# Optimization experiments

Hardware: AMD Instinct MI355X
Metric: run time of the kernel (lower is better)

## Reference

```python
import jax, jax.numpy as jnp
import numpy as np

NEG_SLOPE = 0.2
EPS = 1e-16


def gat_conv(x, edge_index, W, att_src, att_dst, bias, heads, out_ch, concat):
    """PyG GATConv (eval mode, add_self_loops=True).
    x: [N, F_in], edge_index: [2, E] with row0=src(j), row1=dst(i).
    W: [F_in, heads*out_ch], att_src/att_dst: [heads, out_ch], bias: [heads*out_ch] or [out_ch].
    """
    N = x.shape[0]
    loop = jnp.arange(N, dtype=edge_index.dtype)
    src = jnp.concatenate([edge_index[0], loop])
    dst = jnp.concatenate([edge_index[1], loop])

    h = (x @ W).reshape(N, heads, out_ch)                 # [N, H, C]
    a_src = jnp.sum(h * att_src[None], axis=-1)           # [N, H]
    a_dst = jnp.sum(h * att_dst[None], axis=-1)           # [N, H]

    alpha = jax.nn.leaky_relu(a_src[src] + a_dst[dst], NEG_SLOPE)  # [E, H]
    # segment softmax over incoming edges of each destination node
    m = jax.ops.segment_max(alpha, dst, num_segments=N)   # [N, H]
    e = jnp.exp(alpha - m[dst])                           # [E, H]
    s = jax.ops.segment_sum(e, dst, num_segments=N)       # [N, H]
    alpha = e / (s[dst] + EPS)                            # [E, H]

    out = jax.ops.segment_sum(h[src] * alpha[:, :, None], dst, num_segments=N)  # [N, H, C]
    if concat:
        out = out.reshape(N, heads * out_ch)
    else:
        out = out.mean(axis=1)
    return out + bias


def setup_inputs() -> dict:
    key = jax.random.key(0)
    ks = jax.random.split(key, 12)
    N, E, F_in, C = 100000, 1600000, 512, 16
    H1, O1 = 8, 8
    hid = H1 * O1  # 64
    sc1 = 1.0 / np.sqrt(F_in)
    sc2 = 1.0 / np.sqrt(hid)
    return {
        "x": jax.random.normal(ks[0], (N, F_in), jnp.float32),
        "edge_index": jax.random.randint(ks[1], (2, E), 0, N, jnp.int64),
        "W1": jax.random.normal(ks[2], (F_in, hid), jnp.float32) * sc1,
        "att_src1": jax.random.normal(ks[3], (H1, O1), jnp.float32) * sc2,
        "att_dst1": jax.random.normal(ks[4], (H1, O1), jnp.float32) * sc2,
        "bias1": jnp.zeros((hid,), jnp.float32),
        "W2": jax.random.normal(ks[5], (hid, C), jnp.float32) * sc2,
        "att_src2": jax.random.normal(ks[6], (1, C), jnp.float32) * 0.25,
        "att_dst2": jax.random.normal(ks[7], (1, C), jnp.float32) * 0.25,
        "bias2": jnp.zeros((C,), jnp.float32),
    }


def reference(x, edge_index, W1, att_src1, att_dst1, bias1, W2, att_src2, att_dst2, bias2):
    h = gat_conv(x, edge_index, W1, att_src1, att_dst1, bias1, heads=8, out_ch=8, concat=True)
    h = jax.nn.elu(h)
    C = W2.shape[1]
    node_embeddings = gat_conv(h, edge_index, W2, att_src2, att_dst2, bias2, heads=1, out_ch=C, concat=True)
    out = jax.nn.softmax(node_embeddings, axis=-1)
    return (out, node_embeddings)
```

## Files before the change

kernel.cpp:

```cpp
#include <hip/hip_runtime.h>
#include <hip/hip_bf16.h>

#define NEG_SLOPE 0.2f
#define EPSF 1e-16f

typedef __attribute__((ext_vector_type(8))) short bf16x8;
typedef __attribute__((ext_vector_type(4))) float f32x4;

__device__ inline unsigned short f2bf(float x) {
  unsigned int u = __float_as_uint(x);
  return (unsigned short)((u + 0x7fffu + ((u >> 16) & 1u)) >> 16);
}
__device__ inline float bf2f(unsigned short h) {
  return __uint_as_float(((unsigned int)h) << 16);
}

__device__ __forceinline__ void gload16(const void* src, void* dst) {
  __builtin_amdgcn_global_load_lds(
      (const __attribute__((address_space(1))) unsigned int*)src,
      (__attribute__((address_space(3))) unsigned int*)dst, 16, 0, 0);
}

__global__ __launch_bounds__(256) void prep_w_kernel(const float* __restrict__ W,
                                                     unsigned short* __restrict__ wb) {
  int idx = blockIdx.x * 256 + threadIdx.x;
  if (idx >= 512 * 64) return;
  int k = idx >> 6, c = idx & 63;
  float w = W[idx];
  unsigned short h = f2bf(w);
  unsigned short l = f2bf(w - bf2f(h));
  int ch = k >> 5, kin = k & 31;
  int Ap = ((c << 6) + (kin << 1)) ^ ((c & 7) << 4);
  wb[ch * 4096 + (Ap >> 1)] = h;
  wb[ch * 4096 + 2048 + (Ap >> 1)] = l;
}

__global__ __launch_bounds__(256) void gemm1_kernel(const float* __restrict__ x,
                                                    const unsigned short* __restrict__ wb,
                                                    const float* __restrict__ atts,
                                                    const float* __restrict__ attd,
                                                    unsigned short* __restrict__ h1b,
                                                    float* __restrict__ a1s,
                                                    float* __restrict__ a1d, int N) {
  __shared__ __align__(16) float As[3][4096];
  __shared__ __align__(16) unsigned short Bs[3][4096];
  const int tid = threadIdx.x, wv = tid >> 6, lane = tid & 63;
  const int row0 = blockIdx.x * 128;

  const float* asrc[4];
  int aldo[4];
#pragma unroll
  for (int i = 0; i < 4; ++i) {
    int u = i * 256 + wv * 64 + lane;
    int row = u >> 3, w = u & 7;
    int rg = row0 + row;
    if (rg >= N) rg = N - 1;
    asrc[i] = x + (size_t)rg * 512 + ((w ^ (row & 7)) << 2);
    aldo[i] = (i * 256 + wv * 64) * 4;
  }
  const unsigned short* bsrc[2];
  int bldo[2];
#pragma unroll
  for (int i = 0; i < 2; ++i) {
    int u = i * 256 + wv * 64 + lane;
    bsrc[i] = wb + (size_t)u * 8;
    bldo[i] = (i * 256 + wv * 64) * 8;
  }

  const int kofs = (lane >> 4) * 8;
  const int cbase = lane & 15;
  int ardo[2][2];
#pragma unroll
  for (int rt = 0; rt < 2; ++rt) {
    int r = wv * 32 + rt * 16 + cbase;
#pragma unroll
    for (int h = 0; h < 2; ++h)
      ardo[rt][h] = r * 32 + ((((kofs >> 2) + h) ^ (r & 7)) << 2);
  }
  int brdo[4];
#pragma unroll
  for (int ct = 0; ct < 4; ++ct) {
    int c = ct * 16 + cbase;
    brdo[ct] = (((c << 6) + (kofs << 1)) ^ ((c & 7) << 4)) >> 1;
  }

  f32x4 acc[2][4] = {};

  auto stage = [&](int b, int ch) {
#pragma unroll
    for (int i = 0; i < 4; ++i) gload16(asrc[i] + ch * 32, &As[b][aldo[i]]);
#pragma unroll
    for (int i = 0; i < 2; ++i) gload16(bsrc[i] + ch * 4096, &Bs[b][bldo[i]]);
  };

  stage(0, 0);
  stage(1, 1);
  for (int i = 0; i < 16; ++i) {
    const int b = i % 3;
    if (i < 14) {
      stage((i + 2) % 3, i + 2);
      asm volatile("s_waitcnt vmcnt(12)" ::: "memory");
    } else if (i == 14) {
      asm volatile("s_waitcnt vmcnt(6)" ::: "memory");
    } else {
      asm volatile("s_waitcnt vmcnt(0)" ::: "memory");
    }
    __builtin_amdgcn_s_barrier();
    __builtin_amdgcn_sched_barrier(0);

#pragma unroll
    for (int rt = 0; rt < 2; ++rt) {
      float4 a0 = *(const float4*)(&As[b][ardo[rt][0]]);
      float4 a1 = *(const float4*)(&As[b][ardo[rt][1]]);
      float av[8] = {a0.x, a0.y, a0.z, a0.w, a1.x, a1.y, a1.z, a1.w};
      bf16x8 ah, al;
#pragma unroll
      for (int j = 0; j < 8; ++j) {
        unsigned int u = __float_as_uint(av[j]);
        ah[j] = (short)(unsigned short)(u >> 16);
        float lo = av[j] - __uint_as_float(u & 0xffff0000u);
        al[j] = (short)(unsigned short)(__float_as_uint(lo) >> 16);
      }
#pragma unroll
      for (int ct = 0; ct < 4; ++ct) {
        bf16x8 bh = *(const bf16x8*)(&Bs[b][brdo[ct]]);
        bf16x8 bl = *(const bf16x8*)(&Bs[b][brdo[ct] + 2048]);
        acc[rt][ct] = __builtin_amdgcn_mfma_f32_16x16x32_bf16(ah, bh, acc[rt][ct], 0, 0, 0);
        acc[rt][ct] = __builtin_amdgcn_mfma_f32_16x16x32_bf16(al, bh, acc[rt][ct], 0, 0, 0);
        acc[rt][ct] = __builtin_amdgcn_mfma_f32_16x16x32_bf16(ah, bl, acc[rt][ct], 0, 0, 0);
      }
    }
    asm volatile("s_waitcnt lgkmcnt(0)" ::: "memory");
    __builtin_amdgcn_s_barrier();
  }

  float wS[4], wD[4];
#pragma unroll
  for (int ct = 0; ct < 4; ++ct) {
    wS[ct] = atts[ct * 16 + cbase];
    wD[ct] = attd[ct * 16 + cbase];
  }
#pragma unroll
  for (int rt = 0; rt < 2; ++rt) {
#pragma unroll
    for (int ct = 0; ct < 4; ++ct) {
#pragma unroll
      for (int j = 0; j < 4; ++j) {
        int r = row0 + wv * 32 + rt * 16 + (lane >> 4) * 4 + j;
        float a = acc[rt][ct][j];
        if (r < N) h1b[(size_t)r * 64 + ct * 16 + cbase] = f2bf(a);
        float ps = a * wS[ct], pd = a * wD[ct];
        ps += __shfl_xor(ps, 1); pd += __shfl_xor(pd, 1);
        ps += __shfl_xor(ps, 2); pd += __shfl_xor(pd, 2);
        ps += __shfl_xor(ps, 4); pd += __shfl_xor(pd, 4);
        if ((lane & 7) == 0 && r < N) {
          int h = ct * 2 + ((lane >> 3) & 1);
          a1s[r * 8 + h] = ps;
          a1d[r * 8 + h] = pd;
        }
      }
    }
  }
}

__global__ __launch_bounds__(256) void init_deg_kernel(int* __restrict__ deg, int N) {
  int i = blockIdx.x * 256 + threadIdx.x;
  if (i < N) deg[i] = 1;
}

__global__ __launch_bounds__(256) void count_kernel(const int* __restrict__ ei, int E, int* __restrict__ deg) {
  int e = blockIdx.x * 256 + threadIdx.x;
  if (e < E) atomicAdd(&deg[ei[E + e]], 1);
}

__global__ __launch_bounds__(256) void scan1_kernel(int* __restrict__ data, int* __restrict__ blocksum, int N) {
  __shared__ int wave_tot[4];
  int t = threadIdx.x;
  int base = blockIdx.x * 1024;
  int v[4];
  int sum = 0;
#pragma unroll
  for (int i = 0; i < 4; ++i) {
    int idx = base + t * 4 + i;
    v[i] = sum;
    int d = (idx < N) ? data[idx] : 0;
    sum += d;
  }
  int lane = t & 63, wv = t >> 6;
  int x = sum;
#pragma unroll
  for (int ofs = 1; ofs < 64; ofs <<= 1) {
    int y = __shfl_up(x, ofs);
    if (lane >= ofs) x += y;
  }
  if (lane == 63) wave_tot[wv] = x;
  __syncthreads();
  int wofs = 0;
  for (int w = 0; w < wv; ++w) wofs += wave_tot[w];
  int excl_thread = wofs + x - sum;
#pragma unroll
  for (int i = 0; i < 4; ++i) {
    int idx = base + t * 4 + i;
    if (idx < N) data[idx] = excl_thread + v[i];
  }
  if (t == 255) blocksum[blockIdx.x] = wofs + x;
}

__global__ __launch_bounds__(256) void scan2_kernel(int* __restrict__ blocksum, int nb) {
  __shared__ int sm[256];
  int t = threadIdx.x;
  int x = (t < nb) ? blocksum[t] : 0;
  sm[t] = x;
  __syncthreads();
  for (int ofs = 1; ofs < 256; ofs <<= 1) {
    int y = (t >= ofs) ? sm[t - ofs] : 0;
    __syncthreads();
    sm[t] += y;
    __syncthreads();
  }
  if (t < nb) blocksum[t] = sm[t] - x;
}

__global__ __launch_bounds__(256) void scan3_kernel(const int* __restrict__ excl, const int* __restrict__ blocksum,
                                                    int* __restrict__ rowptr, int* __restrict__ cursor,
                                                    int N, int ET) {
  int idx = blockIdx.x * 256 + threadIdx.x;
  if (idx < N) {
    int r = excl[idx] + blocksum[idx >> 10];
    rowptr[idx] = r;
    cursor[idx] = r;
  }
  if (idx == N) rowptr[N] = ET;
}

__global__ __launch_bounds__(256) void scatter_kernel(const int* __restrict__ ei, int E, int ET,
                                                      int* __restrict__ cursor, int* __restrict__ esrc, int N) {
  const int cls = blockIdx.x & 7;
  const int nlo = (int)(((long long)N * cls) >> 3);
  const int nhi = (int)(((long long)N * (cls + 1)) >> 3);
  const int chunk = blockIdx.x >> 3;
  const int nchunks = gridDim.x >> 3;
  const long long stride = (long long)nchunks * 256;
  for (long long e = (long long)chunk * 256 + threadIdx.x; e < ET; e += stride) {
    int s, d;
    if (e < E) { d = ei[E + e]; s = ei[e]; }
    else       { d = (int)(e - E); s = d; }
    if (d >= nlo && d < nhi) {
      int pos = atomicAdd(&cursor[d], 1);
      esrc[pos] = s;
    }
  }
}

__global__ __launch_bounds__(256) void agg1_kernel(const int* __restrict__ rowptr, const int* __restrict__ esrc,
                                                   const float* __restrict__ a1s, const float* __restrict__ a1d,
                                                   const unsigned short* __restrict__ h1b,
                                                   const float* __restrict__ bias1,
                                                   unsigned short* __restrict__ h2b, int N) {
  const int wid = (blockIdx.x * 256 + threadIdx.x) >> 6;
  const int lane = threadIdx.x & 63;
  const int half = lane >> 5, l = lane & 31;
  const int nA = wid * 2;
  if (nA >= N) return;
  const int n = nA + half;
  const bool nvalid = n < N;
  const int nc = nvalid ? n : nA;
  const int h = l >> 2;
  const int c2 = l * 2;

  const float ad = a1d[(unsigned)nc * 8 + h];
  const int beg = rowptr[nc];
  const int deg = nvalid ? (rowptr[nc + 1] - beg) : 0;
  const int degO = __shfl_xor(deg, 32);
  const int dmax = max(deg, degO);
  const int dcl = max(deg, 1) - 1;

  float acc0 = 0.f, acc1 = 0.f, wsum = 0.f;
  for (int it = 0; it < dmax; it += 2) {
    int k0 = beg + min(it, dcl);
    int k1 = beg + min(it + 1, dcl);
    float m0 = (it < deg) ? 1.f : 0.f;
    float m1 = (it + 1 < deg) ? 1.f : 0.f;
    int s0 = esrc[k0], s1 = esrc[k1];
    unsigned int g0 = *(const unsigned int*)(h1b + ((unsigned)s0 * 64 + c2));
    unsigned int g1 = *(const unsigned int*)(h1b + ((unsigned)s1 * 64 + c2));
    float al0 = a1s[(unsigned)s0 * 8 + h] + ad;
    float al1 = a1s[(unsigned)s1 * 8 + h] + ad;
    al0 = fmaxf(al0, NEG_SLOPE * al0);
    al1 = fmaxf(al1, NEG_SLOPE * al1);
    float w0 = __expf(al0) * m0;
    float w1 = __expf(al1) * m1;
    acc0 = fmaf(w0, bf2f((unsigned short)(g0 & 0xffff)), acc0);
    acc1 = fmaf(w0, bf2f((unsigned short)(g0 >> 16)), acc1);
    acc0 = fmaf(w1, bf2f((unsigned short)(g1 & 0xffff)), acc0);
    acc1 = fmaf(w1, bf2f((unsigned short)(g1 >> 16)), acc1);
    wsum += w0 + w1;
  }
  float inv = 1.f / (wsum + EPSF);
  float2 b2 = *(const float2*)(bias1 + c2);
  float v0 = acc0 * inv + b2.x;
  float v1 = acc1 * inv + b2.y;
  v0 = (v0 > 0.f) ? v0 : expm1f(v0);
  v1 = (v1 > 0.f) ? v1 : expm1f(v1);
  if (nvalid) {
    unsigned int pack = (unsigned int)f2bf(v0) | ((unsigned int)f2bf(v1) << 16);
    *(unsigned int*)(h2b + ((unsigned)n * 64 + c2)) = pack;
  }
}

__global__ __launch_bounds__(256) void l2_proj_kernel(const unsigned short* __restrict__ h2b,
                                                      const float* __restrict__ W2,
                                                      const float* __restrict__ atts, const float* __restrict__ attd,
                                                      unsigned short* __restrict__ gb, float* __restrict__ a2s,
                                                      float* __restrict__ a2d, int N) {
  __shared__ float w[1024];
  int tid = threadIdx.x;
  for (int i = tid; i < 1024; i += 256) w[i] = W2[i];
  __syncthreads();
  int gid = blockIdx.x * 256 + tid;
  int n = gid >> 4, c = gid & 15;
  if (n >= N) return;
  const unsigned short* hr = h2b + (size_t)n * 64;
  float acc = 0.f;
#pragma unroll
  for (int k8 = 0; k8 < 8; ++k8) {
    bf16x8 hv = *(const bf16x8*)(hr + k8 * 8);
#pragma unroll
    for (int j = 0; j < 8; ++j)
      acc = fmaf(bf2f((unsigned short)hv[j]), w[(k8 * 8 + j) * 16 + c], acc);
  }
  gb[(size_t)n * 16 + c] = f2bf(acc);
  float ps = acc * atts[c], pd = acc * attd[c];
#pragma unroll
  for (int m = 1; m < 16; m <<= 1) { ps += __shfl_xor(ps, m); pd += __shfl_xor(pd, m); }
  if (c == 0) { a2s[n] = ps; a2d[n] = pd; }
}

__global__ __launch_bounds__(256) void agg2_kernel(const int* __restrict__ rowptr, const int* __restrict__ esrc,
                                                   const float* __restrict__ a2s, const float* __restrict__ a2d,
                                                   const unsigned short* __restrict__ gb,
                                                   const float* __restrict__ bias2,
                                                   float* __restrict__ out_sm, float* __restrict__ emb, int N) {
  int wid = (blockIdx.x * 256 + threadIdx.x) >> 6;
  int lane = threadIdx.x & 63;
  if (wid >= N) return;
  int n = wid;
  int c = lane & 15, sub = lane >> 4;
  float ad = a2d[n];
  int beg = rowptr[n], end = rowptr[n + 1];
  float acc = 0.f, wsum = 0.f;
  for (int k = beg + sub; k < end; k += 4) {
    int s = esrc[k];
    float al = a2s[s] + ad;
    al = fmaxf(al, NEG_SLOPE * al);
    float w = __expf(al);
    acc = fmaf(w, bf2f(gb[(unsigned)s * 16 + c]), acc);
    wsum += w;
  }
  acc += __shfl_xor(acc, 16); acc += __shfl_xor(acc, 32);
  wsum += __shfl_xor(wsum, 16); wsum += __shfl_xor(wsum, 32);
  float v = acc / (wsum + EPSF) + bias2[c];
  float m = v;
#pragma unroll
  for (int k2 = 1; k2 < 16; k2 <<= 1) m = fmaxf(m, __shfl_xor(m, k2));
  float e = __expf(v - m);
  float ssum = e;
#pragma unroll
  for (int k2 = 1; k2 < 16; k2 <<= 1) ssum += __shfl_xor(ssum, k2);
  if (sub == 0) {
    emb[(size_t)n * 16 + c] = v;
    out_sm[(size_t)n * 16 + c] = e / ssum;
  }
}

extern "C" void kernel_launch(void* const* d_in, const int* in_sizes, int n_in,
                              void* d_out, int out_size, void* d_ws, size_t ws_size,
                              hipStream_t stream) {
  const float* x     = (const float*)d_in[0];
  const int*   ei    = (const int*)d_in[1];
  const float* W1    = (const float*)d_in[2];
  const float* atts1 = (const float*)d_in[3];
  const float* attd1 = (const float*)d_in[4];
  const float* bias1 = (const float*)d_in[5];
  const float* W2    = (const float*)d_in[6];
  const float* atts2 = (const float*)d_in[7];
  const float* attd2 = (const float*)d_in[8];
  const float* bias2 = (const float*)d_in[9];

  const int N = in_sizes[0] / 512;
  const int E = in_sizes[1] / 2;
  const int ET = E + N;

  char* wp = (char*)d_ws;
  unsigned short* h1b = (unsigned short*)wp;        wp += (size_t)N * 64 * 2;
  unsigned short* h2b = (unsigned short*)wp;        wp += (size_t)N * 64 * 2;
  float* a1s = (float*)wp;                          wp += (size_t)N * 8 * 4;
  float* a1d = (float*)wp;                          wp += (size_t)N * 8 * 4;
  unsigned short* gb = (unsigned short*)wp;         wp += (size_t)N * 16 * 2;
  float* a2s = (float*)wp;                          wp += (size_t)N * 4;
  float* a2d = (float*)wp;                          wp += (size_t)N * 4;
  int* deg = (int*)wp;                              wp += (size_t)N * 4;
  int* rowptr = (int*)wp;                           wp += (size_t)(N + 1) * 4;
  int* cursor = (int*)wp;                           wp += (size_t)N * 4;
  int* blocksum = (int*)wp;                         wp += 256 * 4;
  int* esrc = (int*)wp;                             wp += (size_t)ET * 4;
  unsigned short* wb = (unsigned short*)wp;         wp += 512 * 64 * 2 * 2;

  float* out_sm = (float*)d_out;
  float* emb    = out_sm + (size_t)N * 16;

  const int nb = (N + 1023) / 1024;

  init_deg_kernel<<<(N + 255) / 256, 256, 0, stream>>>(deg, N);
  count_kernel<<<(E + 255) / 256, 256, 0, stream>>>(ei, E, deg);
  scan1_kernel<<<nb, 256, 0, stream>>>(deg, blocksum, N);
  scan2_kernel<<<1, 256, 0, stream>>>(blocksum, nb);
  scan3_kernel<<<(N + 256) / 256, 256, 0, stream>>>(deg, blocksum, rowptr, cursor, N, ET);
  scatter_kernel<<<8 * 1024, 256, 0, stream>>>(ei, E, ET, cursor, esrc, N);

  prep_w_kernel<<<128, 256, 0, stream>>>(W1, wb);
  gemm1_kernel<<<(N + 127) / 128, 256, 0, stream>>>(x, wb, atts1, attd1, h1b, a1s, a1d, N);
  agg1_kernel<<<(N + 7) / 8, 256, 0, stream>>>(rowptr, esrc, a1s, a1d, h1b, bias1, h2b, N);

  l2_proj_kernel<<<(N * 16 + 255) / 256, 256, 0, stream>>>(h2b, W2, atts2, attd2, gb, a2s, a2d, N);
  agg2_kernel<<<(N + 3) / 4, 256, 0, stream>>>(rowptr, esrc, a2s, a2d, gb, bias2, out_sm, emb, N);
}
```

Baseline: 344.2 us.

## Fuse CSR scatter into GEMM kernel, merge W prep with degree count, pack agg2

Merges the weight bf16-split prep and the in-degree atomic count into one launch. The degree buffer is zeroed with a memset, and the self-loop is added in scan3 as +idx. The edge scatter into CSR now runs as a tail phase of the layer-1 GEMM kernel, so it overlaps with GEMM work across blocks instead of being a separate launch. agg2 now handles two nodes per wavefront, one per half-wave, with masked lockstep iteration to raise lane utilisation. This removes several launches, but it makes the GEMM kernel longer and adds divergent masked work when the two nodes have different degrees.

```diff
diff --git a/kernel.cpp b/kernel.cpp
--- a/kernel.cpp
+++ b/kernel.cpp
@@ -21,27 +21,96 @@
       (__attribute__((address_space(3))) unsigned int*)dst, 16, 0, 0);
 }
 
-__global__ __launch_bounds__(256) void prep_w_kernel(const float* __restrict__ W,
-                                                     unsigned short* __restrict__ wb) {
+__global__ __launch_bounds__(256) void prep_count_kernel(const float* __restrict__ W,
+                                                         unsigned short* __restrict__ wb,
+                                                         int* __restrict__ deg,
+                                                         const int* __restrict__ ei, int E) {
+  const int b = blockIdx.x, tid = threadIdx.x;
+  if (b < 128) {
+    int idx = b * 256 + tid;
+    int k = idx >> 6, c = idx & 63;
+    float w = W[idx];
+    unsigned short h = f2bf(w);
+    unsigned short l = f2bf(w - bf2f(h));
+    int ch = k >> 5, kin = k & 31;
+    int Ap = ((c << 6) + (kin << 1)) ^ ((c & 7) << 4);
+    wb[ch * 4096 + (Ap >> 1)] = h;
+    wb[ch * 4096 + 2048 + (Ap >> 1)] = l;
+  } else {
+    int e = (b - 128) * 256 + tid;
+    if (e < E) atomicAdd(&deg[ei[E + e]], 1);
+  }
+}
+
+__global__ __launch_bounds__(256) void scan1_kernel(int* __restrict__ data, int* __restrict__ blocksum, int N) {
+  __shared__ int wave_tot[4];
+  int t = threadIdx.x;
+  int base = blockIdx.x * 1024;
+  int v[4];
+  int sum = 0;
+#pragma unroll
+  for (int i = 0; i < 4; ++i) {
+    int idx = base + t * 4 + i;
+    v[i] = sum;
+    int d = (idx < N) ? data[idx] : 0;
+    sum += d;
+  }
+  int lane = t & 63, wv = t >> 6;
+  int x = sum;
+#pragma unroll
+  for (int ofs = 1; ofs < 64; ofs <<= 1) {
+    int y = __shfl_up(x, ofs);
+    if (lane >= ofs) x += y;
+  }
+  if (lane == 63) wave_tot[wv] = x;
+  __syncthreads();
+  int wofs = 0;
+  for (int w = 0; w < wv; ++w) wofs += wave_tot[w];
+  int excl_thread = wofs + x - sum;
+#pragma unroll
+  for (int i = 0; i < 4; ++i) {
+    int idx = base + t * 4 + i;
+    if (idx < N) data[idx] = excl_thread + v[i];
+  }
+  if (t == 255) blocksum[blockIdx.x] = wofs + x;
+}
+
+__global__ __launch_bounds__(256) void scan2_kernel(int* __restrict__ blocksum, int nb) {
+  __shared__ int sm[256];
+  int t = threadIdx.x;
+  int x = (t < nb) ? blocksum[t] : 0;
+  sm[t] = x;
+  __syncthreads();
+  for (int ofs = 1; ofs < 256; ofs <<= 1) {
+    int y = (t >= ofs) ? sm[t - ofs] : 0;
+    __syncthreads();
+    sm[t] += y;
+    __syncthreads();
+  }
+  if (t < nb) blocksum[t] = sm[t] - x;
+}
+
+__global__ __launch_bounds__(256) void scan3_kernel(const int* __restrict__ excl, const int* __restrict__ blocksum,
+                                                    int* __restrict__ rowptr, int* __restrict__ cursor,
+                                                    int N, int ET) {
   int idx = blockIdx.x * 256 + threadIdx.x;
-  if (idx >= 512 * 64) return;
-  int k = idx >> 6, c = idx & 63;
-  float w = W[idx];
-  unsigned short h = f2bf(w);
-  unsigned short l = f2bf(w - bf2f(h));
-  int ch = k >> 5, kin = k & 31;
-  int Ap = ((c << 6) + (kin << 1)) ^ ((c & 7) << 4);
-  wb[ch * 4096 + (Ap >> 1)] = h;
-  wb[ch * 4096 + 2048 + (Ap >> 1)] = l;
-}
-
-__global__ __launch_bounds__(256) void gemm1_kernel(const float* __restrict__ x,
-                                                    const unsigned short* __restrict__ wb,
-                                                    const float* __restrict__ atts,
-                                                    const float* __restrict__ attd,
-                                                    unsigned short* __restrict__ h1b,
-                                                    float* __restrict__ a1s,
-                                                    float* __restrict__ a1d, int N) {
+  if (idx < N) {
+    int r = excl[idx] + blocksum[idx >> 10] + idx;
+    rowptr[idx] = r;
+    cursor[idx] = r;
+  }
+  if (idx == N) rowptr[N] = ET;
+}
+
+__global__ __launch_bounds__(256) void mega_kernel(const float* __restrict__ x,
+                                                   const unsigned short* __restrict__ wb,
+                                                   const float* __restrict__ atts,
+                                                   const float* __restrict__ attd,
+                                                   unsigned short* __restrict__ h1b,
+                                                   float* __restrict__ a1s,
+                                                   float* __restrict__ a1d, int N,
+                                                   const int* __restrict__ ei, int E, int ET,
+                                                   int* __restrict__ cursor, int* __restrict__ esrc) {
   __shared__ __align__(16) float As[3][4096];
   __shared__ __align__(16) unsigned short Bs[3][4096];
   const int tid = threadIdx.x, wv = tid >> 6, lane = tid & 63;
@@ -134,120 +203,51 @@
     __builtin_amdgcn_s_barrier();
   }
 
-  float wS[4], wD[4];
-#pragma unroll
-  for (int ct = 0; ct < 4; ++ct) {
-    wS[ct] = atts[ct * 16 + cbase];
-    wD[ct] = attd[ct * 16 + cbase];
-  }
-#pragma unroll
-  for (int rt = 0; rt < 2; ++rt) {
+  {
+    float wS[4], wD[4];
 #pragma unroll
     for (int ct = 0; ct < 4; ++ct) {
-#pragma unroll
-      for (int j = 0; j < 4; ++j) {
-        int r = row0 + wv * 32 + rt * 16 + (lane >> 4) * 4 + j;
-        float a = acc[rt][ct][j];
-        if (r < N) h1b[(size_t)r * 64 + ct * 16 + cbase] = f2bf(a);
-        float ps = a * wS[ct], pd = a * wD[ct];
-        ps += __shfl_xor(ps, 1); pd += __shfl_xor(pd, 1);
-        ps += __shfl_xor(ps, 2); pd += __shfl_xor(pd, 2);
-        ps += __shfl_xor(ps, 4); pd += __shfl_xor(pd, 4);
-        if ((lane & 7) == 0 && r < N) {
-          int h = ct * 2 + ((lane >> 3) & 1);
-          a1s[r * 8 + h] = ps;
-          a1d[r * 8 + h] = pd;
+      wS[ct] = atts[ct * 16 + cbase];
+      wD[ct] = attd[ct * 16 + cbase];
+    }
+#pragma unroll
+    for (int rt = 0; rt < 2; ++rt) {
+#pragma unroll
+      for (int ct = 0; ct < 4; ++ct) {
+#pragma unroll
+        for (int j = 0; j < 4; ++j) {
+          int r = row0 + wv * 32 + rt * 16 + (lane >> 4) * 4 + j;
+          float a = acc[rt][ct][j];
+          if (r < N) h1b[(size_t)r * 64 + ct * 16 + cbase] = f2bf(a);
+          float ps = a * wS[ct], pd = a * wD[ct];
+          ps += __shfl_xor(ps, 1); pd += __shfl_xor(pd, 1);
+          ps += __shfl_xor(ps, 2); pd += __shfl_xor(pd, 2);
+          ps += __shfl_xor(ps, 4); pd += __shfl_xor(pd, 4);
+          if ((lane & 7) == 0 && r < N) {
+            int h = ct * 2 + ((lane >> 3) & 1);
+            a1s[r * 8 + h] = ps;
+            a1d[r * 8 + h] = pd;
+          }
         }
       }
     }
   }
-}
-
-__global__ __launch_bounds__(256) void init_deg_kernel(int* __restrict__ deg, int N) {
-  int i = blockIdx.x * 256 + threadIdx.x;
-  if (i < N) deg[i] = 1;
-}
-
-__global__ __launch_bounds__(256) void count_kernel(const int* __restrict__ ei, int E, int* __restrict__ deg) {
-  int e = blockIdx.x * 256 + threadIdx.x;
-  if (e < E) atomicAdd(&deg[ei[E + e]], 1);
-}
-
-__global__ __launch_bounds__(256) void scan1_kernel(int* __restrict__ data, int* __restrict__ blocksum, int N) {
-  __shared__ int wave_tot[4];
-  int t = threadIdx.x;
-  int base = blockIdx.x * 1024;
-  int v[4];
-  int sum = 0;
-#pragma unroll
-  for (int i = 0; i < 4; ++i) {
-    int idx = base + t * 4 + i;
-    v[i] = sum;
-    int d = (idx < N) ? data[idx] : 0;
-    sum += d;
-  }
-  int lane = t & 63, wv = t >> 6;
-  int x = sum;
-#pragma unroll
-  for (int ofs = 1; ofs < 64; ofs <<= 1) {
-    int y = __shfl_up(x, ofs);
-    if (lane >= ofs) x += y;
-  }
-  if (lane == 63) wave_tot[wv] = x;
-  __syncthreads();
-  int wofs = 0;
-  for (int w = 0; w < wv; ++w) wofs += wave_tot[w];
-  int excl_thread = wofs + x - sum;
-#pragma unroll
-  for (int i = 0; i < 4; ++i) {
-    int idx = base + t * 4 + i;
-    if (idx < N) data[idx] = excl_thread + v[i];
-  }
-  if (t == 255) blocksum[blockIdx.x] = wofs + x;
-}
-
-__global__ __launch_bounds__(256) void scan2_kernel(int* __restrict__ blocksum, int nb) {
-  __shared__ int sm[256];
-  int t = threadIdx.x;
-  int x = (t < nb) ? blocksum[t] : 0;
-  sm[t] = x;
-  __syncthreads();
-  for (int ofs = 1; ofs < 256; ofs <<= 1) {
-    int y = (t >= ofs) ? sm[t - ofs] : 0;
-    __syncthreads();
-    sm[t] += y;
-    __syncthreads();
-  }
-  if (t < nb) blocksum[t] = sm[t] - x;
-}
-
-__global__ __launch_bounds__(256) void scan3_kernel(const int* __restrict__ excl, const int* __restrict__ blocksum,
-                                                    int* __restrict__ rowptr, int* __restrict__ cursor,
-                                                    int N, int ET) {
-  int idx = blockIdx.x * 256 + threadIdx.x;
-  if (idx < N) {
-    int r = excl[idx] + blocksum[idx >> 10];
-    rowptr[idx] = r;
-    cursor[idx] = r;
-  }
-  if (idx == N) rowptr[N] = ET;
-}
-
-__global__ __launch_bounds__(256) void scatter_kernel(const int* __restrict__ ei, int E, int ET,
-                                                      int* __restrict__ cursor, int* __restrict__ esrc, int N) {
-  const int cls = blockIdx.x & 7;
-  const int nlo = (int)(((long long)N * cls) >> 3);
-  const int nhi = (int)(((long long)N * (cls + 1)) >> 3);
-  const int chunk = blockIdx.x >> 3;
-  const int nchunks = gridDim.x >> 3;
-  const long long stride = (long long)nchunks * 256;
-  for (long long e = (long long)chunk * 256 + threadIdx.x; e < ET; e += stride) {
-    int s, d;
-    if (e < E) { d = ei[E + e]; s = ei[e]; }
-    else       { d = (int)(e - E); s = d; }
-    if (d >= nlo && d < nhi) {
-      int pos = atomicAdd(&cursor[d], 1);
-      esrc[pos] = s;
+
+  {
+    const int cls = blockIdx.x & 7;
+    const int nlo = (int)(((long long)N * cls) >> 3);
+    const int nhi = (int)(((long long)N * (cls + 1)) >> 3);
+    const int chunk = blockIdx.x >> 3;
+    const int nch = ((int)gridDim.x - cls + 7) >> 3;
+    const long long stride = (long long)nch * 256;
+    for (long long e = (long long)chunk * 256 + tid; e < ET; e += stride) {
+      int s, d;
+      if (e < E) { d = ei[E + e]; s = ei[e]; }
+      else       { d = (int)(e - E); s = d; }
+      if (d >= nlo && d < nhi) {
+        int pos = atomicAdd(&cursor[d], 1);
+        esrc[pos] = s;
+      }
     }
   }
 }
@@ -341,33 +341,45 @@
                                                    const unsigned short* __restrict__ gb,
                                                    const float* __restrict__ bias2,
                                                    float* __restrict__ out_sm, float* __restrict__ emb, int N) {
-  int wid = (blockIdx.x * 256 + threadIdx.x) >> 6;
-  int lane = threadIdx.x & 63;
-  if (wid >= N) return;
-  int n = wid;
-  int c = lane & 15, sub = lane >> 4;
-  float ad = a2d[n];
-  int beg = rowptr[n], end = rowptr[n + 1];
+  const int wid = (blockIdx.x * 256 + threadIdx.x) >> 6;
+  const int lane = threadIdx.x & 63;
+  const int half = lane >> 5, l = lane & 31;
+  const int nA = wid * 2;
+  if (nA >= N) return;
+  const int n = nA + half;
+  const bool nvalid = n < N;
+  const int nc = nvalid ? n : nA;
+  const int c = l & 15, sub = l >> 4;
+
+  const float ad = a2d[nc];
+  const int beg = rowptr[nc];
+  const int deg = nvalid ? (rowptr[nc + 1] - beg) : 0;
+  const int degO = __shfl_xor(deg, 32);
+  const int dmax = max(deg, degO);
+  const int dcl = max(deg, 1) - 1;
+
   float acc = 0.f, wsum = 0.f;
-  for (int k = beg + sub; k < end; k += 4) {
+  for (int it = 0; it < dmax; it += 2) {
+    int k = beg + min(it + sub, dcl);
+    float m = (it + sub < deg) ? 1.f : 0.f;
     int s = esrc[k];
     float al = a2s[s] + ad;
     al = fmaxf(al, NEG_SLOPE * al);
-    float w = __expf(al);
+    float w = __expf(al) * m;
     acc = fmaf(w, bf2f(gb[(unsigned)s * 16 + c]), acc);
     wsum += w;
   }
-  acc += __shfl_xor(acc, 16); acc += __shfl_xor(acc, 32);
-  wsum += __shfl_xor(wsum, 16); wsum += __shfl_xor(wsum, 32);
+  acc += __shfl_xor(acc, 16);
+  wsum += __shfl_xor(wsum, 16);
   float v = acc / (wsum + EPSF) + bias2[c];
-  float m = v;
-#pragma unroll
-  for (int k2 = 1; k2 < 16; k2 <<= 1) m = fmaxf(m, __shfl_xor(m, k2));
-  float e = __expf(v - m);
+  float mx = v;
+#pragma unroll
+  for (int k2 = 1; k2 < 16; k2 <<= 1) mx = fmaxf(mx, __shfl_xor(mx, k2));
+  float e = __expf(v - mx);
   float ssum = e;
 #pragma unroll
   for (int k2 = 1; k2 < 16; k2 <<= 1) ssum += __shfl_xor(ssum, k2);
-  if (sub == 0) {
+  if (sub == 0 && nvalid) {
     emb[(size_t)n * 16 + c] = v;
     out_sm[(size_t)n * 16 + c] = e / ssum;
   }
@@ -410,18 +422,18 @@
   float* emb    = out_sm + (size_t)N * 16;
 
   const int nb = (N + 1023) / 1024;
-
-  init_deg_kernel<<<(N + 255) / 256, 256, 0, stream>>>(deg, N);
-  count_kernel<<<(E + 255) / 256, 256, 0, stream>>>(ei, E, deg);
+  const int nCnt = (E + 255) / 256;
+
+  hipMemsetAsync(deg, 0, (size_t)N * sizeof(int), stream);
+  prep_count_kernel<<<128 + nCnt, 256, 0, stream>>>(W1, wb, deg, ei, E);
   scan1_kernel<<<nb, 256, 0, stream>>>(deg, blocksum, N);
   scan2_kernel<<<1, 256, 0, stream>>>(blocksum, nb);
   scan3_kernel<<<(N + 256) / 256, 256, 0, stream>>>(deg, blocksum, rowptr, cursor, N, ET);
-  scatter_kernel<<<8 * 1024, 256, 0, stream>>>(ei, E, ET, cursor, esrc, N);
-
-  prep_w_kernel<<<128, 256, 0, stream>>>(W1, wb);
-  gemm1_kernel<<<(N + 127) / 128, 256, 0, stream>>>(x, wb, atts1, attd1, h1b, a1s, a1d, N);
+
+  mega_kernel<<<(N + 127) / 128, 256, 0, stream>>>(x, wb, atts1, attd1, h1b, a1s, a1d, N,
+                                                   ei, E, ET, cursor, esrc);
+
   agg1_kernel<<<(N + 7) / 8, 256, 0, stream>>>(rowptr, esrc, a1s, a1d, h1b, bias1, h2b, N);
-
   l2_proj_kernel<<<(N * 16 + 255) / 256, 256, 0, stream>>>(h2b, W2, atts2, attd2, gb, a2s, a2d, N);
-  agg2_kernel<<<(N + 3) / 4, 256, 0, stream>>>(rowptr, esrc, a2s, a2d, gb, bias2, out_sm, emb, N);
-}
+  agg2_kernel<<<(N + 7) / 8, 256, 0, stream>>>(rowptr, esrc, a2s, a2d, gb, bias2, out_sm, emb, N);
+}
```

Measured after the change: 377.3 us. 9.6% more time.
